# Kernel tuning notes

Hardware: AMD Instinct MI355X
Metric: run time of the kernel (lower is better)

The kernel has to match this reference:

```python
import jax, jax.numpy as jnp
import numpy as np

B, CIN, HID, T, W, H, TAU = 8, 16, 64, 4, 32, 32, 5
EPS = 1e-5
DN = ('NCDHW', 'OIDHW', 'NCDHW')


def conv3d(x, w, b):
    # 'same' conv3d, NCDHW layout
    y = jax.lax.conv_general_dilated(x, w, (1, 1, 1), 'SAME', dimension_numbers=DN)
    return y + b[None, :, None, None, None]


def ln3(u):
    # F.layer_norm over the last 3 (spatial) dims, no affine
    mu = jnp.mean(u, axis=(-3, -2, -1), keepdims=True)
    var = jnp.var(u, axis=(-3, -2, -1), keepdims=True)
    return (u - mu) * jax.lax.rsqrt(var + EPS)


def ln4(u, w, b):
    # nn.LayerNorm(memory_shape): over last 4 dims (C,T,W,H), with affine
    mu = jnp.mean(u, axis=(-4, -3, -2, -1), keepdims=True)
    var = jnp.var(u, axis=(-4, -3, -2, -1), keepdims=True)
    return (u - mu) * jax.lax.rsqrt(var + EPS) * w + b


def self_attention(r, c_history):
    scale = 1.0 / np.sqrt(T * W * H)
    scores = jnp.einsum('bctwh,lbctwh->bl', r, c_history) * scale  # [B, TAU]
    # faithful to source: softmax over dim=0 (the batch axis of the [b,l] scores)
    attn = jax.nn.softmax(scores, axis=0)
    return jnp.einsum('bl,lbctwh->bctwh', attn, c_history)


def setup_inputs() -> dict:
    key = jax.random.key(0)
    ks = jax.random.split(key, 8)
    x = jax.random.normal(ks[0], (B, CIN, T, W, H), jnp.float32)
    c_history = jax.random.normal(ks[1], (TAU, B, HID, T, W, H), jnp.float32)
    m = jax.random.normal(ks[2], (B, HID, T, W, H), jnp.float32)
    h = jax.random.normal(ks[3], (B, HID, T, W, H), jnp.float32)
    Wx = jax.random.normal(ks[4], (7, HID, CIN, 3, 3, 3), jnp.float32) * 0.05
    bx = jnp.zeros((7, HID), jnp.float32)
    # 9 state-branch conv kernels: [hr, hi, hg, mi', mg', mf', ho, co, mo]
    Wh = jax.random.normal(ks[5], (9, HID, HID, 3, 3, 3), jnp.float32) * 0.02
    bh = jnp.zeros((9, HID), jnp.float32)
    w111 = jax.random.normal(ks[6], (HID, 2 * HID, 1, 1, 1), jnp.float32) * 0.05
    b111 = jnp.zeros((HID,), jnp.float32)
    ln_w = jnp.ones((HID, T, W, H), jnp.float32)
    ln_b = jnp.zeros((HID, T, W, H), jnp.float32)
    return dict(x=x, c_history=c_history, m=m, h=h, Wx=Wx, bx=bx, Wh=Wh, bh=bh,
                w111=w111, b111=b111, ln_w=ln_w, ln_b=ln_b)


def reference(x, c_history, m, h, Wx, bx, Wh, bh, w111, b111, ln_w, ln_b):
    cx = lambda i: conv3d(x, Wx[i], bx[i])
    cs = lambda u, i: conv3d(u, Wh[i], bh[i])
    r = jax.nn.sigmoid(ln3(cx(0) + cs(h, 0)))
    i = jax.nn.sigmoid(ln3(cx(1) + cs(h, 1)))
    g = jnp.tanh(ln3(cx(2) + cs(h, 2)))
    recall = self_attention(r, c_history)
    c = i * g + ln4(c_history[-1] + recall, ln_w, ln_b)
    i_p = jax.nn.sigmoid(ln3(cx(3) + cs(m, 3)))
    g_p = jnp.tanh(ln3(cx(4) + cs(m, 4)))
    f_p = jax.nn.sigmoid(ln3(cx(5) + cs(m, 5)))
    m_new = i_p * g_p + f_p * m
    o = jax.nn.sigmoid(ln3(cx(6) + cs(h, 6) + cs(c, 7) + cs(m_new, 8)))
    h_new = o * jnp.tanh(conv3d(jnp.concatenate([c, m_new], axis=1), w111, b111))
    c_history_new = jnp.concatenate([c_history[1:], c[None]], axis=0)
    return (c_history_new, m_new, h_new)
```

## Files before the change

kernel.cpp:

```cpp
#include <hip/hip_runtime.h>
#include <hip/hip_bf16.h>
#include <math.h>

#define BATCH 8
#define CIN 16
#define HID 64
#define S2 1024
#define SP 4096
#define CHB 262144
#define TAU 5
#define GATE_SZ 2097152
#define EPS 1e-5f

#define WS_Z_OFF   ((size_t)3 * GATE_SZ)
#define WS_ST_OFF  ((size_t)4 * GATE_SZ)

typedef unsigned short u16;
typedef __attribute__((ext_vector_type(8))) short  short8;
typedef __attribute__((ext_vector_type(8))) u16    ushort8;
typedef __attribute__((ext_vector_type(4))) float  f32x4;

#define N7 (7*27*64*96)
#define NO (27*64*128)
#define N1 (64*128)

__device__ __forceinline__ u16 f2b(float v) {
    __hip_bfloat16 h = __float2bfloat16(v);
    u16 r; __builtin_memcpy(&r, &h, 2); return r;
}

__device__ __forceinline__ float* gate_ptr(float* out, float* ws, int g) {
    return (g < 4) ? (out + (size_t)g * GATE_SZ) : (ws + (size_t)(g - 4) * GATE_SZ);
}

__global__ __launch_bounds__(256) void pack_w_k(const float* __restrict__ Wx,
                                                const float* __restrict__ Wh,
                                                const float* __restrict__ w111,
                                                u16* __restrict__ A7, u16* __restrict__ Ao,
                                                u16* __restrict__ A111,
                                                float* __restrict__ stats)
{
    if (blockIdx.x == 0 && threadIdx.x < 128) stats[threadIdx.x] = 0.f;
    const int idx = blockIdx.x * 256 + threadIdx.x;
    if (idx < N7) {
        const int k = idx % 96, oc = (idx / 96) % 64, tap = (idx / (96*64)) % 27, g = idx / (96*64*27);
        float v = 0.f;
        if (k < 16)      v = Wx[((size_t)(g*64 + oc)*16 + k)      * 27 + tap];
        else if (k < 80) v = Wh[((size_t)(g*64 + oc)*64 + (k-16)) * 27 + tap];
        A7[idx] = f2b(v);
    } else if (idx < N7 + NO) {
        const int j = idx - N7;
        const int k = j % 128, oc = (j / 128) % 64, tap = j / (128*64);
        float v = (k < 64) ? Wh[((size_t)(7*64 + oc)*64 + k)      * 27 + tap]
                           : Wh[((size_t)(8*64 + oc)*64 + (k-64)) * 27 + tap];
        Ao[j] = f2b(v);
    } else if (idx < N7 + NO + N1) {
        const int j = idx - N7 - NO;
        A111[j] = f2b(w111[j]);
    }
}

__global__ __launch_bounds__(256) void pack_xhm_k(const float* __restrict__ x,
                                                  const float* __restrict__ h,
                                                  const float* __restrict__ m,
                                                  u16* __restrict__ XH, u16* __restrict__ XM)
{
    __shared__ float t[144][65];
    const int bi = blockIdx.x, b = bi >> 6, s0 = (bi & 63) << 6;
    for (int i = threadIdx.x; i < 144*64; i += 256) {
        const int row = i >> 6, sc = i & 63;
        float v;
        if (row < 16)      v = x[((size_t)b*16 + row)      * SP + s0 + sc];
        else if (row < 80) v = h[((size_t)b*64 + (row-16)) * SP + s0 + sc];
        else               v = m[((size_t)b*64 + (row-80)) * SP + s0 + sc];
        t[row][sc] = v;
    }
    __syncthreads();
    for (int j = threadIdx.x; j < 64*96; j += 256) {
        const int s = j / 96, ch = j % 96;
        const size_t o = ((size_t)b*4096 + s0 + s) * 96 + ch;
        XH[o] = f2b(ch < 80 ? t[ch][s] : 0.f);
        XM[o] = f2b(ch < 16 ? t[ch][s] : (ch < 80 ? t[ch + 64][s] : 0.f));
    }
}

__device__ __forceinline__ int swz32(int r, int c) {
    return r * 32 + ((c ^ ((r >> 1) & 3)) << 3);
}

template<int KCH, int TAPS, int NR, int MODE>
__global__ __launch_bounds__(256, 3) void conv_mfma_k(
    const u16* __restrict__ XA, const u16* __restrict__ XB,
    const u16* __restrict__ Apack,
    const float* __restrict__ bxp, const float* __restrict__ bhp,
    const float* __restrict__ b111,
    float* __restrict__ out, float* __restrict__ ws)
{
    constexpr int YT   = NR + 2;
    constexpr int ROWS = 4 * YT * 34;
    constexpr int PADK = 32;
    __shared__ __align__(16) u16 xs[ROWS * PADK];

    const int bi = blockIdx.x;
    int g = 0, b, y0, kc_lo = 0, kc_hi = KCH / 32;
    const u16* X; const u16* Ag; float* outp;
    if (MODE == 0) {
        constexpr int YB = 32 / NR;
        g  = bi / (8 * YB);
        b  = (bi / YB) % 8;
        y0 = (bi % YB) * NR;
        X  = (g >= 3 && g <= 5) ? XB : XA;
        Ag = Apack + (size_t)g * TAPS * 64 * KCH;
        outp = gate_ptr(out, ws, g) + (size_t)b * CHB;
    } else if (MODE == 1) {
        b = bi >> 5; y0 = bi & 31;
        X = XA; Ag = Apack;
        outp = ws + (size_t)2 * GATE_SZ + (size_t)b * CHB;
    } else {
        b = bi >> 5; y0 = bi & 31;
        X = XA; Ag = Apack;
        outp = ws + (size_t)b * CHB;
    }
    const u16* Xb = X + (size_t)b * 4096 * KCH;

    const int tid  = threadIdx.x;
    const int w    = tid >> 6;
    const int lane = tid & 63;
    const int xn   = lane & 15, quad = lane >> 4;

    f32x4 acc[4][2 * NR] = {};

    for (int kc = kc_lo; kc < kc_hi; ++kc) {
        if (kc != kc_lo) __syncthreads();
        for (int cix = tid; cix < ROWS * 4; cix += 256) {
            const int r = cix >> 2, sub = cix & 3;
            const int t = r / (YT * 34), rem = r % (YT * 34);
            const int yy = rem / 34, xx = rem % 34;
            const int gy = y0 + yy - 1, gx = xx - 1;
            ushort8 v = {0, 0, 0, 0, 0, 0, 0, 0};
            if ((unsigned)gy < 32u && (unsigned)gx < 32u)
                v = *(const ushort8*)&Xb[(size_t)(t * 1024 + gy * 32 + gx) * KCH + kc * 32 + sub * 8];
            *(ushort8*)&xs[swz32(r, sub)] = v;
        }
        __syncthreads();

        auto load_a = [&](short8* a, int tap) {
            #pragma unroll
            for (int mt = 0; mt < 4; ++mt)
                a[mt] = *(const short8*)&Ag[(size_t)(tap * 64 + mt * 16 + xn) * KCH + kc * 32 + quad * 8];
        };
        auto load_b = [&](short8* bf, int tap) {
            int kd, ky, kx;
            if (TAPS == 27) { kd = tap / 9; ky = (tap / 3) % 3; kx = tap % 3; }
            else            { kd = 1; ky = 1; kx = 1; }
            const int tin = w + kd - 1;
            #pragma unroll
            for (int nt = 0; nt < 2 * NR; ++nt) {
                const int ysub = nt >> 1, xh = nt & 1;
                const int row = (tin * YT + ysub + ky) * 34 + xh * 16 + xn + kx;
                bf[nt] = *(const short8*)&xs[swz32(row, quad)];
            }
        };
        auto do_mfma = [&](short8* a, short8* bf) {
            #pragma unroll
            for (int nt = 0; nt < 2 * NR; ++nt)
                #pragma unroll
                for (int mt = 0; mt < 4; ++mt)
                    acc[mt][nt] = __builtin_amdgcn_mfma_f32_16x16x32_bf16(a[mt], bf[nt], acc[mt][nt], 0, 0, 0);
        };

        if (TAPS == 27) {
            const int tap_lo = (w == 0) ? 9 : 0;
            const int tap_hi = (w == 3) ? 18 : 27;
            short8 a0[4], b0[2 * NR], a1[4], b1[2 * NR];
            load_a(a0, tap_lo); load_b(b0, tap_lo);
            int tap = tap_lo;
            for (; tap + 2 <= tap_hi; tap += 2) {
                load_a(a1, tap + 1); load_b(b1, tap + 1);
                do_mfma(a0, b0);
                if (tap + 2 < tap_hi) { load_a(a0, tap + 2); load_b(b0, tap + 2); }
                do_mfma(a1, b1);
            }
            if (tap < tap_hi) do_mfma(a0, b0);
        } else {
            short8 a0[4], b0[2 * NR];
            load_a(a0, 0); load_b(b0, 0);
            do_mfma(a0, b0);
        }
    }

    #pragma unroll
    for (int mt = 0; mt < 4; ++mt)
    #pragma unroll
    for (int nt = 0; nt < 2 * NR; ++nt) {
        const int ysub = nt >> 1, xh = nt & 1;
        const int sp = w * 1024 + (y0 + ysub) * 32 + xh * 16 + xn;
        #pragma unroll
        for (int reg = 0; reg < 4; ++reg) {
            const int oc = mt * 16 + quad * 4 + reg;
            float bias;
            if (MODE == 0)      bias = bxp[g * 64 + oc] + bhp[g * 64 + oc];
            else if (MODE == 1) bias = bhp[7 * 64 + oc] + bhp[8 * 64 + oc];
            else                bias = b111[oc];
            float* p = outp + (size_t)oc * SP + sp;
            float vv = acc[mt][nt][reg] + bias;
            if (MODE == 1) vv += *p;
            *p = vv;
        }
    }
}

__global__ __launch_bounds__(256) void ln3_act_k(float* __restrict__ out,
                                                 float* __restrict__ ws, int gate0)
{
    const int blk = blockIdx.x;
    const int g = gate0 + (blk >> 9);
    float* p = gate_ptr(out, ws, g) + (size_t)(blk & 511) * SP;
    const int tid = threadIdx.x;

    float s = 0.f, s2 = 0.f;
    for (int k = tid; k < SP; k += 256) { float v = p[k]; s += v; s2 += v * v; }
    #pragma unroll
    for (int off = 32; off > 0; off >>= 1) { s += __shfl_down(s, off); s2 += __shfl_down(s2, off); }
    __shared__ float rs[4], rs2[4], stat[2];
    if ((tid & 63) == 0) { rs[tid >> 6] = s; rs2[tid >> 6] = s2; }
    __syncthreads();
    if (tid == 0) {
        float S  = rs[0] + rs[1] + rs[2] + rs[3];
        float Sq = rs2[0] + rs2[1] + rs2[2] + rs2[3];
        float mu  = S * (1.f / SP);
        float var = Sq * (1.f / SP) - mu * mu;
        stat[0] = mu; stat[1] = rsqrtf(var + EPS);
    }
    __syncthreads();
    const float mu = stat[0], r = stat[1];
    const bool use_tanh = (g == 2 || g == 4);
    for (int k = tid; k < SP; k += 256) {
        float v = (p[k] - mu) * r;
        p[k] = use_tanh ? tanhf(v) : 1.f / (1.f + expf(-v));
    }
}

__global__ __launch_bounds__(256) void scores_k(const float* __restrict__ r,
                                                const float* __restrict__ chist,
                                                float* __restrict__ stats)
{
    const int blk = blockIdx.x;
    const int b = blk >> 6, chunk = blk & 63;
    const float* rp = r + (size_t)b * CHB;
    const int lo = chunk * (CHB / 64);
    float s[TAU] = {};
    for (int k = lo + threadIdx.x; k < lo + CHB / 64; k += 256) {
        const float rv = rp[k];
        #pragma unroll
        for (int l = 0; l < TAU; ++l) s[l] += rv * chist[(size_t)(l * BATCH + b) * CHB + k];
    }
    __shared__ float rsh[TAU][4];
    #pragma unroll
    for (int l = 0; l < TAU; ++l) {
        float v = s[l];
        #pragma unroll
        for (int off = 32; off > 0; off >>= 1) v += __shfl_down(v, off);
        if ((threadIdx.x & 63) == 0) rsh[l][threadIdx.x >> 6] = v;
    }
    __syncthreads();
    if (threadIdx.x < TAU) {
        const int l = threadIdx.x;
        atomicAdd(&stats[l * 8 + b],
                  (rsh[l][0] + rsh[l][1] + rsh[l][2] + rsh[l][3]) * (1.f / 64.f));
    }
}

__global__ __launch_bounds__(256) void recall_k(const float* __restrict__ chist,
                                                float* __restrict__ ws,
                                                float* __restrict__ part)
{
    const float* stats = ws + WS_ST_OFF;
    const int blk = blockIdx.x;
    const int b = blk >> 10;
    const int idx = (blk & 1023) * 256 + threadIdx.x;

    __shared__ float attn[TAU];
    if (threadIdx.x < TAU) {
        const int l = threadIdx.x;
        float mx = -1e30f;
        for (int bb = 0; bb < BATCH; ++bb) mx = fmaxf(mx, stats[l * 8 + bb]);
        float sum = 0.f, e = 0.f;
        for (int bb = 0; bb < BATCH; ++bb) {
            float t = expf(stats[l * 8 + bb] - mx);
            sum += t;
            if (bb == b) e = t;
        }
        attn[l] = e / sum;
    }
    __syncthreads();
    const float a0 = attn[0], a1 = attn[1], a2 = attn[2], a3 = attn[3], a4 = attn[4];

    const size_t e = (size_t)b * CHB + idx;
    const size_t LB = (size_t)BATCH * CHB;
    float z = chist[4 * LB + e] * (1.f + a4)
            + a0 * chist[0 * LB + e] + a1 * chist[1 * LB + e]
            + a2 * chist[2 * LB + e] + a3 * chist[3 * LB + e];
    ws[WS_Z_OFF + e] = z;

    float s = z, s2 = z * z;
    #pragma unroll
    for (int off = 32; off > 0; off >>= 1) { s += __shfl_down(s, off); s2 += __shfl_down(s2, off); }
    __shared__ float rs[4], rs2[4];
    if ((threadIdx.x & 63) == 0) { rs[threadIdx.x >> 6] = s; rs2[threadIdx.x >> 6] = s2; }
    __syncthreads();
    if (threadIdx.x == 0) {
        part[blk]        = rs[0] + rs[1] + rs[2] + rs[3];
        part[8192 + blk] = rs2[0] + rs2[1] + rs2[2] + rs2[3];
    }
}

__global__ __launch_bounds__(256) void cm_pcm_k(float* __restrict__ out, float* __restrict__ ws,
                                                const float* __restrict__ m,
                                                const float* __restrict__ lnw,
                                                const float* __restrict__ lnb,
                                                const float* __restrict__ part,
                                                u16* __restrict__ PCM)
{
    __shared__ __align__(16) u16 tl[64][136];
    const int bi = blockIdx.x;
    const int b = bi >> 6;
    const int s0 = (bi & 63) << 6;

    float s = 0.f, s2 = 0.f;
    for (int j = threadIdx.x; j < 1024; j += 256) {
        s  += part[b * 1024 + j];
        s2 += part[8192 + b * 1024 + j];
    }
    #pragma unroll
    for (int off = 32; off > 0; off >>= 1) { s += __shfl_down(s, off); s2 += __shfl_down(s2, off); }
    __shared__ float rs[4], rs2[4], st[2];
    if ((threadIdx.x & 63) == 0) { rs[threadIdx.x >> 6] = s; rs2[threadIdx.x >> 6] = s2; }
    __syncthreads();
    if (threadIdx.x == 0) {
        float S  = rs[0] + rs[1] + rs[2] + rs[3];
        float Sq = rs2[0] + rs2[1] + rs2[2] + rs2[3];
        float mu  = S * (1.f / CHB);
        float var = Sq * (1.f / CHB) - mu * mu;
        st[0] = mu; st[1] = rsqrtf(var + EPS);
    }
    __syncthreads();
    const float mu = st[0], rstd = st[1];

    for (int i = threadIdx.x; i < 1024; i += 256) {
        const int chn = i >> 4;
        const int sp4 = (i & 15) << 2;
        const size_t e = (size_t)b * CHB + (size_t)chn * SP + s0 + sp4;
        const size_t le = (size_t)chn * SP + s0 + sp4;
        float4 z  = *(const float4*)&ws[WS_Z_OFF + e];
        float4 gi = *(const float4*)&gate_ptr(out, ws, 1)[e];
        float4 gg = *(const float4*)&gate_ptr(out, ws, 2)[e];
        float4 ip = *(const float4*)&gate_ptr(out, ws, 3)[e];
        float4 gp = *(const float4*)&gate_ptr(out, ws, 4)[e];
        float4 fp = *(const float4*)&gate_ptr(out, ws, 5)[e];
        float4 mm = *(const float4*)&m[e];
        float4 lw = *(const float4*)&lnw[le];
        float4 lb = *(const float4*)&lnb[le];
        float4 c, mn;
        c.x = gi.x * gg.x + (z.x - mu) * rstd * lw.x + lb.x;
        c.y = gi.y * gg.y + (z.y - mu) * rstd * lw.y + lb.y;
        c.z = gi.z * gg.z + (z.z - mu) * rstd * lw.z + lb.z;
        c.w = gi.w * gg.w + (z.w - mu) * rstd * lw.w + lb.w;
        mn.x = ip.x * gp.x + fp.x * mm.x;
        mn.y = ip.y * gp.y + fp.y * mm.y;
        mn.z = ip.z * gp.z + fp.z * mm.z;
        mn.w = ip.w * gp.w + fp.w * mm.w;
        *(float4*)&out[(size_t)4 * GATE_SZ + e] = c;
        *(float4*)&out[(size_t)5 * GATE_SZ + e] = mn;
        const float cc[4] = {c.x, c.y, c.z, c.w};
        const float mm2[4] = {mn.x, mn.y, mn.z, mn.w};
        #pragma unroll
        for (int k = 0; k < 4; ++k) {
            tl[sp4 + k][chn]      = f2b(cc[k]);
            tl[sp4 + k][64 + chn] = f2b(mm2[k]);
        }
    }
    __syncthreads();
    for (int j = threadIdx.x; j < 1024; j += 256) {
        const int sidx = j >> 4, c8 = (j & 15) << 3;
        ushort8 v = *(const ushort8*)&tl[sidx][c8];
        *(ushort8*)&PCM[((size_t)b * 4096 + s0 + sidx) * 128 + c8] = v;
    }
}

__global__ __launch_bounds__(256) void tail_k(const float* __restrict__ chist,
                                              const float* __restrict__ o,
                                              const float* __restrict__ v,
                                              float* __restrict__ out)
{
    const int bi = blockIdx.x;
    if (bi < 8192) {
        const size_t i = (size_t)bi * 256 + threadIdx.x;
        ((float4*)out)[i] = ((const float4*)(chist + GATE_SZ))[i];
    } else {
        const size_t i = (size_t)(bi - 8192) * 256 + threadIdx.x;
        float4 ov = ((const float4*)o)[i], vv = ((const float4*)v)[i];
        float4 r;
        r.x = ov.x * tanhf(vv.x); r.y = ov.y * tanhf(vv.y);
        r.z = ov.z * tanhf(vv.z); r.w = ov.w * tanhf(vv.w);
        ((float4*)(out + (size_t)6 * GATE_SZ))[i] = r;
    }
}

extern "C" void kernel_launch(void* const* d_in, const int* in_sizes, int n_in,
                              void* d_out, int out_size, void* d_ws, size_t ws_size,
                              hipStream_t stream)
{
    const float* x    = (const float*)d_in[0];
    const float* ch   = (const float*)d_in[1];
    const float* m    = (const float*)d_in[2];
    const float* h    = (const float*)d_in[3];
    const float* Wx   = (const float*)d_in[4];
    const float* bx   = (const float*)d_in[5];
    const float* Wh   = (const float*)d_in[6];
    const float* bh   = (const float*)d_in[7];
    const float* w111 = (const float*)d_in[8];
    const float* b111 = (const float*)d_in[9];
    const float* lnw  = (const float*)d_in[10];
    const float* lnb  = (const float*)d_in[11];
    float* out = (float*)d_out;
    float* ws  = (float*)d_ws;

    u16* XH   = (u16*)(out + (size_t)4 * GATE_SZ);
    u16* A7   = (u16*)(out + (size_t)5 * GATE_SZ);
    u16* XM   = (u16*)(out + (size_t)6 * GATE_SZ);
    u16* Ao   = XM + (size_t)BATCH * 4096 * 96;
    u16* A111 = Ao + (size_t)NO;
    u16* PCM  = (u16*)out;
    float* part  = (float*)(A111 + N1);
    float* stats = ws + WS_ST_OFF;

    pack_w_k<<<(N7 + NO + N1 + 255) / 256, 256, 0, stream>>>(Wx, Wh, w111, A7, Ao, A111, stats);
    pack_xhm_k<<<512, 256, 0, stream>>>(x, h, m, XH, XM);

    conv_mfma_k<96, 27, 2, 0><<<896, 256, 0, stream>>>(XH, XM, A7, bx, bh, nullptr, out, ws);
    ln3_act_k<<<3072, 256, 0, stream>>>(out, ws, 0);

    scores_k<<<512, 256, 0, stream>>>(out, ch, stats);
    recall_k<<<8192, 256, 0, stream>>>(ch, ws, part);
    cm_pcm_k<<<512, 256, 0, stream>>>(out, ws, m, lnw, lnb, part, PCM);

    conv_mfma_k<128, 27, 1, 1><<<256, 256, 0, stream>>>(PCM, nullptr, Ao, nullptr, bh, nullptr, out, ws);
    ln3_act_k<<<512, 256, 0, stream>>>(out, ws, 6);
    conv_mfma_k<128, 1, 1, 2><<<256, 256, 0, stream>>>(PCM, nullptr, A111, nullptr, nullptr, b111, out, ws);

    tail_k<<<10240, 256, 0, stream>>>(ch, ws + (size_t)2 * GATE_SZ, ws, out);
}
```

Measured before the change: 398.3 us.

## Defer gate activations into consumers, simplify conv tap loop, use fast math

The LN3 pass over the first six gates now only computes per-channel mean/rstd into a small stats buffer. The normalisation and sigmoid/tanh are applied on the fly in the scores and cell/memory-combining kernels, which removes a full read-modify-write pass over six gate tensors. The conv kernel drops its manual two-stage register double-buffering for a simpler kd/ky/kx loop and raises the occupancy hint from 3 to 4 waves per SIMD. Fast __expf-based sigmoid/tanh replace the libm calls, at some accuracy cost; the register cap could also cause spills.

```diff
diff --git a/kernel.cpp b/kernel.cpp
--- a/kernel.cpp
+++ b/kernel.cpp
@@ -31,6 +31,16 @@
 
 __device__ __forceinline__ float* gate_ptr(float* out, float* ws, int g) {
     return (g < 4) ? (out + (size_t)g * GATE_SZ) : (ws + (size_t)(g - 4) * GATE_SZ);
+}
+
+__device__ __forceinline__ float fsig(float v) {
+    v = fminf(fmaxf(v, -30.f), 30.f);
+    return 1.f / (1.f + __expf(-v));
+}
+__device__ __forceinline__ float ftanh(float v) {
+    v = fminf(fmaxf(v, -15.f), 15.f);
+    const float t = __expf(-2.f * v);
+    return (1.f - t) / (1.f + t);
 }
 
 __global__ __launch_bounds__(256) void pack_w_k(const float* __restrict__ Wx,
@@ -89,7 +99,7 @@
 }
 
 template<int KCH, int TAPS, int NR, int MODE>
-__global__ __launch_bounds__(256, 3) void conv_mfma_k(
+__global__ __launch_bounds__(256, 4) void conv_mfma_k(
     const u16* __restrict__ XA, const u16* __restrict__ XB,
     const u16* __restrict__ Apack,
     const float* __restrict__ bxp, const float* __restrict__ bhp,
@@ -98,8 +108,7 @@
 {
     constexpr int YT   = NR + 2;
     constexpr int ROWS = 4 * YT * 34;
-    constexpr int PADK = 32;
-    __shared__ __align__(16) u16 xs[ROWS * PADK];
+    __shared__ __align__(16) u16 xs[ROWS * 32];
 
     const int bi = blockIdx.x;
     int g = 0, b, y0, kc_lo = 0, kc_hi = KCH / 32;
@@ -144,48 +153,49 @@
         }
         __syncthreads();
 
-        auto load_a = [&](short8* a, int tap) {
+        if (TAPS == 27) {
+            const int kd_lo = (w == 0) ? 1 : 0;
+            const int kd_hi = (w == 3) ? 2 : 3;
+            for (int kd = kd_lo; kd < kd_hi; ++kd) {
+                const int tin  = w + kd - 1;
+                const int rowt = tin * YT * 34;
+                #pragma unroll
+                for (int jj = 0; jj < 9; ++jj) {
+                    const int ky = jj / 3, kx = jj % 3;
+                    short8 a[4], bf[2 * NR];
+                    #pragma unroll
+                    for (int mt = 0; mt < 4; ++mt)
+                        a[mt] = *(const short8*)
+                            &Ag[(size_t)((kd * 9 + jj) * 64 + mt * 16 + xn) * KCH + kc * 32 + quad * 8];
+                    #pragma unroll
+                    for (int nt = 0; nt < 2 * NR; ++nt) {
+                        const int ysub = nt >> 1, xh = nt & 1;
+                        const int row = rowt + (ysub + ky) * 34 + xh * 16 + xn + kx;
+                        bf[nt] = *(const short8*)&xs[swz32(row, quad)];
+                    }
+                    #pragma unroll
+                    for (int nt = 0; nt < 2 * NR; ++nt)
+                        #pragma unroll
+                        for (int mt = 0; mt < 4; ++mt)
+                            acc[mt][nt] = __builtin_amdgcn_mfma_f32_16x16x32_bf16(a[mt], bf[nt], acc[mt][nt], 0, 0, 0);
+                }
+            }
+        } else {
+            short8 a[4], bf[2 * NR];
             #pragma unroll
             for (int mt = 0; mt < 4; ++mt)
-                a[mt] = *(const short8*)&Ag[(size_t)(tap * 64 + mt * 16 + xn) * KCH + kc * 32 + quad * 8];
-        };
-        auto load_b = [&](short8* bf, int tap) {
-            int kd, ky, kx;
-            if (TAPS == 27) { kd = tap / 9; ky = (tap / 3) % 3; kx = tap % 3; }
-            else            { kd = 1; ky = 1; kx = 1; }
-            const int tin = w + kd - 1;
+                a[mt] = *(const short8*)&Ag[(size_t)(mt * 16 + xn) * KCH + kc * 32 + quad * 8];
             #pragma unroll
             for (int nt = 0; nt < 2 * NR; ++nt) {
                 const int ysub = nt >> 1, xh = nt & 1;
-                const int row = (tin * YT + ysub + ky) * 34 + xh * 16 + xn + kx;
+                const int row = (w * YT + ysub + 1) * 34 + xh * 16 + xn + 1;
                 bf[nt] = *(const short8*)&xs[swz32(row, quad)];
             }
-        };
-        auto do_mfma = [&](short8* a, short8* bf) {
             #pragma unroll
             for (int nt = 0; nt < 2 * NR; ++nt)
                 #pragma unroll
                 for (int mt = 0; mt < 4; ++mt)
                     acc[mt][nt] = __builtin_amdgcn_mfma_f32_16x16x32_bf16(a[mt], bf[nt], acc[mt][nt], 0, 0, 0);
-        };
-
-        if (TAPS == 27) {
-            const int tap_lo = (w == 0) ? 9 : 0;
-            const int tap_hi = (w == 3) ? 18 : 27;
-            short8 a0[4], b0[2 * NR], a1[4], b1[2 * NR];
-            load_a(a0, tap_lo); load_b(b0, tap_lo);
-            int tap = tap_lo;
-            for (; tap + 2 <= tap_hi; tap += 2) {
-                load_a(a1, tap + 1); load_b(b1, tap + 1);
-                do_mfma(a0, b0);
-                if (tap + 2 < tap_hi) { load_a(a0, tap + 2); load_b(b0, tap + 2); }
-                do_mfma(a1, b1);
-            }
-            if (tap < tap_hi) do_mfma(a0, b0);
-        } else {
-            short8 a0[4], b0[2 * NR];
-            load_a(a0, 0); load_b(b0, 0);
-            do_mfma(a0, b0);
         }
     }
 
@@ -210,6 +220,32 @@
     }
 }
 
+__global__ __launch_bounds__(256) void ln3_stats_k(float* __restrict__ out,
+                                                   float* __restrict__ ws,
+                                                   float* __restrict__ lnstats)
+{
+    const int blk = blockIdx.x;
+    const int g = blk >> 9;
+    const float* p = gate_ptr(out, ws, g) + (size_t)(blk & 511) * SP;
+    const int tid = threadIdx.x;
+
+    float s = 0.f, s2 = 0.f;
+    for (int k = tid; k < SP; k += 256) { float v = p[k]; s += v; s2 += v * v; }
+    #pragma unroll
+    for (int off = 32; off > 0; off >>= 1) { s += __shfl_down(s, off); s2 += __shfl_down(s2, off); }
+    __shared__ float rs[4], rs2[4];
+    if ((tid & 63) == 0) { rs[tid >> 6] = s; rs2[tid >> 6] = s2; }
+    __syncthreads();
+    if (tid == 0) {
+        float S  = rs[0] + rs[1] + rs[2] + rs[3];
+        float Sq = rs2[0] + rs2[1] + rs2[2] + rs2[3];
+        float mu  = S * (1.f / SP);
+        float var = Sq * (1.f / SP) - mu * mu;
+        lnstats[2 * blk]     = mu;
+        lnstats[2 * blk + 1] = rsqrtf(var + EPS);
+    }
+}
+
 __global__ __launch_bounds__(256) void ln3_act_k(float* __restrict__ out,
                                                  float* __restrict__ ws, int gate0)
 {
@@ -234,24 +270,24 @@
     }
     __syncthreads();
     const float mu = stat[0], r = stat[1];
-    const bool use_tanh = (g == 2 || g == 4);
-    for (int k = tid; k < SP; k += 256) {
-        float v = (p[k] - mu) * r;
-        p[k] = use_tanh ? tanhf(v) : 1.f / (1.f + expf(-v));
-    }
-}
-
-__global__ __launch_bounds__(256) void scores_k(const float* __restrict__ r,
+    for (int k = tid; k < SP; k += 256)
+        p[k] = fsig((p[k] - mu) * r);
+}
+
+__global__ __launch_bounds__(256) void scores_k(const float* __restrict__ u0,
                                                 const float* __restrict__ chist,
+                                                const float* __restrict__ lnstats,
                                                 float* __restrict__ stats)
 {
     const int blk = blockIdx.x;
-    const int b = blk >> 6, chunk = blk & 63;
-    const float* rp = r + (size_t)b * CHB;
-    const int lo = chunk * (CHB / 64);
+    const int b = blk >> 6, chn = blk & 63;
+    const float mu = lnstats[2 * (b * 64 + chn)];
+    const float rr = lnstats[2 * (b * 64 + chn) + 1];
+    const float* rp = u0 + (size_t)b * CHB;
+    const int lo = chn * SP;
     float s[TAU] = {};
-    for (int k = lo + threadIdx.x; k < lo + CHB / 64; k += 256) {
-        const float rv = rp[k];
+    for (int k = lo + threadIdx.x; k < lo + SP; k += 256) {
+        const float rv = fsig((rp[k] - mu) * rr);
         #pragma unroll
         for (int l = 0; l < TAU; ++l) s[l] += rv * chist[(size_t)(l * BATCH + b) * CHB + k];
     }
@@ -287,7 +323,7 @@
         for (int bb = 0; bb < BATCH; ++bb) mx = fmaxf(mx, stats[l * 8 + bb]);
         float sum = 0.f, e = 0.f;
         for (int bb = 0; bb < BATCH; ++bb) {
-            float t = expf(stats[l * 8 + bb] - mx);
+            float t = __expf(stats[l * 8 + bb] - mx);
             sum += t;
             if (bb == b) e = t;
         }
@@ -320,13 +356,20 @@
                                                 const float* __restrict__ lnw,
                                                 const float* __restrict__ lnb,
                                                 const float* __restrict__ part,
+                                                const float* __restrict__ lnstats,
                                                 u16* __restrict__ PCM)
 {
     __shared__ __align__(16) u16 tl[64][136];
+    __shared__ float lst[5][64][2];
     const int bi = blockIdx.x;
     const int b = bi >> 6;
     const int s0 = (bi & 63) << 6;
 
+    for (int j = threadIdx.x; j < 5 * 64; j += 256) {
+        const int gg = j >> 6, chn = j & 63;
+        lst[gg][chn][0] = lnstats[2 * ((gg + 1) * 512 + b * 64 + chn)];
+        lst[gg][chn][1] = lnstats[2 * ((gg + 1) * 512 + b * 64 + chn) + 1];
+    }
     float s = 0.f, s2 = 0.f;
     for (int j = threadIdx.x; j < 1024; j += 256) {
         s  += part[b * 1024 + j];
@@ -353,32 +396,48 @@
         const size_t e = (size_t)b * CHB + (size_t)chn * SP + s0 + sp4;
         const size_t le = (size_t)chn * SP + s0 + sp4;
         float4 z  = *(const float4*)&ws[WS_Z_OFF + e];
-        float4 gi = *(const float4*)&gate_ptr(out, ws, 1)[e];
-        float4 gg = *(const float4*)&gate_ptr(out, ws, 2)[e];
-        float4 ip = *(const float4*)&gate_ptr(out, ws, 3)[e];
-        float4 gp = *(const float4*)&gate_ptr(out, ws, 4)[e];
-        float4 fp = *(const float4*)&gate_ptr(out, ws, 5)[e];
+        float4 u1 = *(const float4*)&gate_ptr(out, ws, 1)[e];
+        float4 u2 = *(const float4*)&gate_ptr(out, ws, 2)[e];
+        float4 u3 = *(const float4*)&gate_ptr(out, ws, 3)[e];
+        float4 u4 = *(const float4*)&gate_ptr(out, ws, 4)[e];
+        float4 u5 = *(const float4*)&gate_ptr(out, ws, 5)[e];
         float4 mm = *(const float4*)&m[e];
         float4 lw = *(const float4*)&lnw[le];
         float4 lb = *(const float4*)&lnb[le];
+        const float m1 = lst[0][chn][0], r1 = lst[0][chn][1];
+        const float m2 = lst[1][chn][0], r2 = lst[1][chn][1];
+        const float m3 = lst[2][chn][0], r3 = lst[2][chn][1];
+        const float m4 = lst[3][chn][0], r4 = lst[3][chn][1];
+        const float m5 = lst[4][chn][0], r5 = lst[4][chn][1];
         float4 c, mn;
-        c.x = gi.x * gg.x + (z.x - mu) * rstd * lw.x + lb.x;
-        c.y = gi.y * gg.y + (z.y - mu) * rstd * lw.y + lb.y;
-        c.z = gi.z * gg.z + (z.z - mu) * rstd * lw.z + lb.z;
-        c.w = gi.w * gg.w + (z.w - mu) * rstd * lw.w + lb.w;
-        mn.x = ip.x * gp.x + fp.x * mm.x;
-        mn.y = ip.y * gp.y + fp.y * mm.y;
-        mn.z = ip.z * gp.z + fp.z * mm.z;
-        mn.w = ip.w * gp.w + fp.w * mm.w;
+        {
+            const float uu1[4] = {u1.x, u1.y, u1.z, u1.w};
+            const float uu2[4] = {u2.x, u2.y, u2.z, u2.w};
+            const float uu3[4] = {u3.x, u3.y, u3.z, u3.w};
+            const float uu4[4] = {u4.x, u4.y, u4.z, u4.w};
+            const float uu5[4] = {u5.x, u5.y, u5.z, u5.w};
+            const float zz[4]  = {z.x, z.y, z.z, z.w};
+            const float mmv[4] = {mm.x, mm.y, mm.z, mm.w};
+            const float lwv[4] = {lw.x, lw.y, lw.z, lw.w};
+            const float lbv[4] = {lb.x, lb.y, lb.z, lb.w};
+            float cv[4], mv[4];
+            #pragma unroll
+            for (int k = 0; k < 4; ++k) {
+                const float gi = fsig ((uu1[k] - m1) * r1);
+                const float gg = ftanh((uu2[k] - m2) * r2);
+                const float ip = fsig ((uu3[k] - m3) * r3);
+                const float gp = ftanh((uu4[k] - m4) * r4);
+                const float fp = fsig ((uu5[k] - m5) * r5);
+                cv[k] = gi * gg + (zz[k] - mu) * rstd * lwv[k] + lbv[k];
+                mv[k] = ip * gp + fp * mmv[k];
+                tl[sp4 + k][chn]      = f2b(cv[k]);
+                tl[sp4 + k][64 + chn] = f2b(mv[k]);
+            }
+            c.x = cv[0]; c.y = cv[1]; c.z = cv[2]; c.w = cv[3];
+            mn.x = mv[0]; mn.y = mv[1]; mn.z = mv[2]; mn.w = mv[3];
+        }
         *(float4*)&out[(size_t)4 * GATE_SZ + e] = c;
         *(float4*)&out[(size_t)5 * GATE_SZ + e] = mn;
-        const float cc[4] = {c.x, c.y, c.z, c.w};
-        const float mm2[4] = {mn.x, mn.y, mn.z, mn.w};
-        #pragma unroll
-        for (int k = 0; k < 4; ++k) {
-            tl[sp4 + k][chn]      = f2b(cc[k]);
-            tl[sp4 + k][64 + chn] = f2b(mm2[k]);
-        }
     }
     __syncthreads();
     for (int j = threadIdx.x; j < 1024; j += 256) {
@@ -401,8 +460,8 @@
         const size_t i = (size_t)(bi - 8192) * 256 + threadIdx.x;
         float4 ov = ((const float4*)o)[i], vv = ((const float4*)v)[i];
         float4 r;
-        r.x = ov.x * tanhf(vv.x); r.y = ov.y * tanhf(vv.y);
-        r.z = ov.z * tanhf(vv.z); r.w = ov.w * tanhf(vv.w);
+        r.x = ov.x * ftanh(vv.x); r.y = ov.y * ftanh(vv.y);
+        r.z = ov.z * ftanh(vv.z); r.w = ov.w * ftanh(vv.w);
         ((float4*)(out + (size_t)6 * GATE_SZ))[i] = r;
     }
 }
@@ -432,18 +491,19 @@
     u16* Ao   = XM + (size_t)BATCH * 4096 * 96;
     u16* A111 = Ao + (size_t)NO;
     u16* PCM  = (u16*)out;
-    float* part  = (float*)(A111 + N1);
-    float* stats = ws + WS_ST_OFF;
+    float* part    = (float*)(A111 + N1);
+    float* lnstats = part + 16384;
+    float* stats   = ws + WS_ST_OFF;
 
     pack_w_k<<<(N7 + NO + N1 + 255) / 256, 256, 0, stream>>>(Wx, Wh, w111, A7, Ao, A111, stats);
     pack_xhm_k<<<512, 256, 0, stream>>>(x, h, m, XH, XM);
 
     conv_mfma_k<96, 27, 2, 0><<<896, 256, 0, stream>>>(XH, XM, A7, bx, bh, nullptr, out, ws);
-    ln3_act_k<<<3072, 256, 0, stream>>>(out, ws, 0);
-
-    scores_k<<<512, 256, 0, stream>>>(out, ch, stats);
+    ln3_stats_k<<<3072, 256, 0, stream>>>(out, ws, lnstats);
+
+    scores_k<<<512, 256, 0, stream>>>(out, ch, lnstats, stats);
     recall_k<<<8192, 256, 0, stream>>>(ch, ws, part);
-    cm_pcm_k<<<512, 256, 0, stream>>>(out, ws, m, lnw, lnb, part, PCM);
+    cm_pcm_k<<<512, 256, 0, stream>>>(out, ws, m, lnw, lnb, part, lnstats, PCM);
 
     conv_mfma_k<128, 27, 1, 1><<<256, 256, 0, stream>>>(PCM, nullptr, Ao, nullptr, bh, nullptr, out, ws);
     ln3_act_k<<<512, 256, 0, stream>>>(out, ws, 6);
```

After: 479.5 us. +20.4%, slower.
